# Optimization experiments

Measured on AMD Instinct MI355X. Metric: run time of the kernel, lower is better.

## Reference

```python
import math
import jax, jax.numpy as jnp
import numpy as np

B, CK, H, W = 4, 64, 48, 84


def setup_inputs() -> dict:
    key = jax.random.key(0)
    k1, k2 = jax.random.split(key)
    mk = jax.random.normal(k1, (B, CK, 1, H, W), dtype=jnp.float32)
    qk = jax.random.normal(k2, (B, CK, H, W), dtype=jnp.float32)
    return {"mk": mk, "qk": qk}


def reference(mk, qk):
    b_, ck = mk.shape[0], mk.shape[1]
    mkf = mk.reshape(b_, ck, -1)            # [B, CK, N]  (N = T*H*W, T=1)
    qkf = qk.reshape(b_, ck, -1)            # [B, CK, M]  (M = H*W)
    a = jnp.sum(mkf * mkf, axis=1)[:, :, None]              # [B, N, 1]
    b = 2.0 * jnp.einsum('bcn,bcm->bnm', mkf, qkf)          # [B, N, M]
    c = jnp.sum(qkf * qkf, axis=1)[:, None, :]              # [B, 1, M]
    affinity = (-a + b - c) / math.sqrt(ck)                 # -||mk - qk||^2 / sqrt(CK)
    return jax.nn.softmax(affinity, axis=1)                 # softmax over memory axis
```

## Files before the change

kernel.cpp:

```cpp
#include <hip/hip_runtime.h>
#include <math.h>

#define B_  4
#define CK_ 64
#define N_  4032
#define M_  4032
#define NP_ 4096
#define MP_ 4096

#define P1C 8
#define P1T 8
#define P2G 8
#define P2T 8

typedef __attribute__((ext_vector_type(8))) short short8;
typedef __attribute__((ext_vector_type(4))) float float4v;

__device__ inline unsigned short f2bf(float x) {
    unsigned u = __float_as_uint(x);
    u += 0x7FFF + ((u >> 16) & 1);
    return (unsigned short)(u >> 16);
}
__device__ inline float bf2f(unsigned short h) {
    return __uint_as_float(((unsigned)h) << 16);
}

__global__ __launch_bounds__(256) void prep_kernel(
    const float* __restrict__ mk, const float* __restrict__ qk,
    unsigned short* __restrict__ mk_hi, unsigned short* __restrict__ mk_lo,
    unsigned short* __restrict__ qk_hi, unsigned short* __restrict__ qk_lo,
    float* __restrict__ u)
{
    __shared__ float tile[64][65];
    __shared__ float sred[4][64];
    const int t  = threadIdx.x;
    const int n0 = blockIdx.x * 64;
    const int b  = blockIdx.y;
    const int which = blockIdx.z;
    const bool pad = (n0 >= N_);

    const float* src = (which == 0 ? mk : qk) + (size_t)b * CK_ * N_;
    unsigned short* dhi = (which == 0 ? mk_hi : qk_hi) + (size_t)b * NP_ * CK_;
    unsigned short* dlo = (which == 0 ? mk_lo : qk_lo) + (size_t)b * NP_ * CK_;

    if (!pad) {
        #pragma unroll
        for (int i = 0; i < 16; ++i) {
            const int idx = t + 256 * i;
            const int c = idx >> 6, n = idx & 63;
            tile[c][n] = src[(size_t)c * N_ + n0 + n];
        }
    } else {
        #pragma unroll
        for (int i = 0; i < 16; ++i) {
            const int idx = t + 256 * i;
            tile[idx >> 6][idx & 63] = 0.f;
        }
    }
    __syncthreads();

    const int n = t & 63;
    const int g = t >> 6;
    unsigned short hbits[16], lbits[16];
    float ssq = 0.f;
    #pragma unroll
    for (int i = 0; i < 16; ++i) {
        const float x = tile[g * 16 + i][n];
        const unsigned short h = f2bf(x);
        hbits[i] = h;
        lbits[i] = f2bf(x - bf2f(h));
        ssq = fmaf(x, x, ssq);
    }
    {
        union { short8 v; unsigned short s[8]; } p0, p1, q0, q1;
        #pragma unroll
        for (int i = 0; i < 8; ++i) {
            p0.s[i] = hbits[i]; p1.s[i] = hbits[8 + i];
            q0.s[i] = lbits[i]; q1.s[i] = lbits[8 + i];
        }
        const size_t base = (size_t)(n0 + n) * CK_ + g * 16;
        *(short8*)(dhi + base)     = p0.v;
        *(short8*)(dhi + base + 8) = p1.v;
        *(short8*)(dlo + base)     = q0.v;
        *(short8*)(dlo + base + 8) = q1.v;
    }
    sred[g][n] = ssq;
    __syncthreads();
    if (which == 0 && t < 64) {
        const float tot = sred[0][t] + sred[1][t] + sred[2][t] + sred[3][t];
        u[(size_t)b * NP_ + n0 + t] = pad ? 0.f : __expf(-0.125f * tot);
    }
}


__global__ __launch_bounds__(512) void pass1_kernel(
    const unsigned short* __restrict__ mk_hi, const unsigned short* __restrict__ mk_lo,
    const unsigned short* __restrict__ qk_hi, const unsigned short* __restrict__ qk_lo,
    const float* __restrict__ u, float* __restrict__ psum)
{
    __shared__ float cs[2][128];
    const int t = threadIdx.x;
    const int wave = t >> 6, lane = t & 63;
    const int wn = wave & 1, wm = wave >> 1;
    const int lcol = lane & 15;
    const int quad = lane >> 4;
    const int chunk = blockIdx.y;
    const int b = blockIdx.z;
    const int m_base = blockIdx.x * 128 + wm * 32;

    const unsigned short* mh = mk_hi + (size_t)b * NP_ * CK_;
    const unsigned short* ml = mk_lo + (size_t)b * NP_ * CK_;
    const unsigned short* qh = qk_hi + (size_t)b * NP_ * CK_;
    const unsigned short* ql = qk_lo + (size_t)b * NP_ * CK_;
    const float* ub = u + (size_t)b * NP_;

    short8 bh[2][2], bl[2][2];
    #pragma unroll
    for (int cg = 0; cg < 2; ++cg) {
        const size_t mrow = (size_t)(m_base + cg * 16 + lcol) * CK_;
        #pragma unroll
        for (int kc = 0; kc < 2; ++kc) {
            const size_t off = mrow + kc * 32 + quad * 8;
            bh[cg][kc] = *(const short8*)(qh + off);
            bl[cg][kc] = *(const short8*)(ql + off);
        }
    }

    float p0 = 0.f, p1 = 0.f;

    #pragma unroll 2
    for (int it = chunk * P1T; it < chunk * P1T + P1T; ++it) {
        const int n_base = it * 64 + wn * 32;
        short8 ah[2][2], al[2][2];
        #pragma unroll
        for (int rg = 0; rg < 2; ++rg) {
            const size_t nrow = (size_t)(n_base + rg * 16 + lcol) * CK_;
            #pragma unroll
            for (int kc = 0; kc < 2; ++kc) {
                const size_t off = nrow + kc * 32 + quad * 8;
                ah[rg][kc] = *(const short8*)(mh + off);
                al[rg][kc] = *(const short8*)(ml + off);
            }
        }
        float4v uv0 = *(const float4v*)(ub + n_base + quad * 4);
        float4v uv1 = *(const float4v*)(ub + n_base + 16 + quad * 4);

        #pragma unroll
        for (int rg = 0; rg < 2; ++rg) {
            #pragma unroll
            for (int cg = 0; cg < 2; ++cg) {
                float4v a1 = {0.f, 0.f, 0.f, 0.f};
                float4v a2 = {0.f, 0.f, 0.f, 0.f};
                __builtin_amdgcn_s_setprio(1);
                #pragma unroll
                for (int kc = 0; kc < 2; ++kc) {
                    a1 = __builtin_amdgcn_mfma_f32_16x16x32_bf16(ah[rg][kc], bh[cg][kc], a1, 0, 0, 0);
                    a2 = __builtin_amdgcn_mfma_f32_16x16x32_bf16(ah[rg][kc], bl[cg][kc], a2, 0, 0, 0);
                    a2 = __builtin_amdgcn_mfma_f32_16x16x32_bf16(al[rg][kc], bh[cg][kc], a2, 0, 0, 0);
                }
                __builtin_amdgcn_s_setprio(0);
                float ps = 0.f;
                #pragma unroll
                for (int r = 0; r < 4; ++r) {
                    const float dot = a1[r] + a2[r];
                    const float uvr = (rg == 0) ? uv0[r] : uv1[r];
                    ps += uvr * __expf(0.25f * dot);
                }
                if (cg == 0) p0 += ps; else p1 += ps;
            }
        }
    }

    p0 += __shfl_xor(p0, 16); p0 += __shfl_xor(p0, 32);
    p1 += __shfl_xor(p1, 16); p1 += __shfl_xor(p1, 32);
    if (lane < 16) {
        cs[wn][wm * 32 + lcol]      = p0;
        cs[wn][wm * 32 + 16 + lcol] = p1;
    }
    __syncthreads();
    if (t < 128) {
        psum[((size_t)b * P1C + chunk) * MP_ + blockIdx.x * 128 + t] =
            cs[0][t] + cs[1][t];
    }
}

__global__ __launch_bounds__(512) void pass2_kernel(
    const unsigned short* __restrict__ mk_hi, const unsigned short* __restrict__ mk_lo,
    const unsigned short* __restrict__ qk_hi, const unsigned short* __restrict__ qk_lo,
    const float* __restrict__ u, const float* __restrict__ psum,
    float* __restrict__ out)
{
    const int t = threadIdx.x;
    const int wave = t >> 6, lane = t & 63;
    const int wn = wave & 1, wm = wave >> 1;
    const int lcol = lane & 15;
    const int quad = lane >> 4;
    const int b = blockIdx.z;
    const int m_base = blockIdx.x * 128 + wm * 32;

    const unsigned short* mh = mk_hi + (size_t)b * NP_ * CK_;
    const unsigned short* ml = mk_lo + (size_t)b * NP_ * CK_;
    const unsigned short* qh = qk_hi + (size_t)b * NP_ * CK_;
    const unsigned short* ql = qk_lo + (size_t)b * NP_ * CK_;
    const float* ub = u + (size_t)b * NP_;

    short8 qah[2][2], qal[2][2];
    #pragma unroll
    for (int mg = 0; mg < 2; ++mg) {
        const size_t mrow = (size_t)(m_base + mg * 16 + lcol) * CK_;
        #pragma unroll
        for (int kc = 0; kc < 2; ++kc) {
            const size_t off = mrow + kc * 32 + quad * 8;
            qah[mg][kc] = *(const short8*)(qh + off);
            qal[mg][kc] = *(const short8*)(ql + off);
        }
    }

    float4v rinv4[2];
    #pragma unroll
    for (int mg = 0; mg < 2; ++mg) {
        float4v tot = {0.f, 0.f, 0.f, 0.f};
        #pragma unroll
        for (int c = 0; c < P1C; ++c) {
            const float4v p = *(const float4v*)(
                psum + ((size_t)b * P1C + c) * MP_ + m_base + mg * 16 + quad * 4);
            tot += p;
        }
        rinv4[mg][0] = 1.f / tot[0];
        rinv4[mg][1] = 1.f / tot[1];
        rinv4[mg][2] = 1.f / tot[2];
        rinv4[mg][3] = 1.f / tot[3];
    }

    const bool mval0 = (m_base < N_);
    const bool mval1 = (m_base + 16 < N_);

    float* obase = out + (size_t)b * N_ * M_ + m_base + quad * 4;

    #pragma unroll 2
    for (int j = 0; j < P2T; ++j) {
        const int n_base = (blockIdx.y * P2T + j) * 64 + wn * 32;

        short8 bh[2][2], bl[2][2];
        #pragma unroll
        for (int ng = 0; ng < 2; ++ng) {
            const size_t nrow = (size_t)(n_base + ng * 16 + lcol) * CK_;
            #pragma unroll
            for (int kc = 0; kc < 2; ++kc) {
                const size_t off = nrow + kc * 32 + quad * 8;
                bh[ng][kc] = *(const short8*)(mh + off);
                bl[ng][kc] = *(const short8*)(ml + off);
            }
        }
        float un[2];
        #pragma unroll
        for (int ng = 0; ng < 2; ++ng)
            un[ng] = ub[n_base + ng * 16 + lcol];

        const bool nval = (n_base < N_);

        #pragma unroll
        for (int mg = 0; mg < 2; ++mg) {
            #pragma unroll
            for (int ng = 0; ng < 2; ++ng) {
                float4v a1 = {0.f, 0.f, 0.f, 0.f};
                float4v a2 = {0.f, 0.f, 0.f, 0.f};
                __builtin_amdgcn_s_setprio(1);
                #pragma unroll
                for (int kc = 0; kc < 2; ++kc) {
                    a1 = __builtin_amdgcn_mfma_f32_16x16x32_bf16(qah[mg][kc], bh[ng][kc], a1, 0, 0, 0);
                    a2 = __builtin_amdgcn_mfma_f32_16x16x32_bf16(qah[mg][kc], bl[ng][kc], a2, 0, 0, 0);
                    a2 = __builtin_amdgcn_mfma_f32_16x16x32_bf16(qal[mg][kc], bh[ng][kc], a2, 0, 0, 0);
                }
                __builtin_amdgcn_s_setprio(0);
                float4v v;
                #pragma unroll
                for (int r = 0; r < 4; ++r) {
                    const float dot = a1[r] + a2[r];
                    v[r] = un[ng] * __expf(0.25f * dot) * rinv4[mg][r];
                }
                if (nval && (mg == 0 ? mval0 : mval1)) {
                    float4v* dst = (float4v*)(
                        obase + (size_t)(n_base + ng * 16 + lcol) * M_ + mg * 16);
                    __builtin_nontemporal_store(v, dst);
                }
            }
        }
    }
}

extern "C" void kernel_launch(void* const* d_in, const int* in_sizes, int n_in,
                              void* d_out, int out_size, void* d_ws, size_t ws_size,
                              hipStream_t stream) {
    const float* mk = (const float*)d_in[0];
    const float* qk = (const float*)d_in[1];
    float* out = (float*)d_out;

    unsigned short* mk_hi = (unsigned short*)d_ws;
    unsigned short* mk_lo = mk_hi + (size_t)B_ * NP_ * CK_;
    unsigned short* qk_hi = mk_lo + (size_t)B_ * NP_ * CK_;
    unsigned short* qk_lo = qk_hi + (size_t)B_ * NP_ * CK_;
    float* u    = (float*)(qk_lo + (size_t)B_ * NP_ * CK_);
    float* psum = u + (size_t)B_ * NP_;

    prep_kernel<<<dim3(NP_ / 64, B_, 2), 256, 0, stream>>>(mk, qk, mk_hi, mk_lo, qk_hi, qk_lo, u);
    pass1_kernel<<<dim3(MP_ / 128, P1C, B_), 512, 0, stream>>>(mk_hi, mk_lo, qk_hi, qk_lo, u, psum);
    pass2_kernel<<<dim3(MP_ / 128, P2G, B_), 512, 0, stream>>>(mk_hi, mk_lo, qk_hi, qk_lo, u, psum, out);
}
```

Measured before the change: 377.2 us.

## Fuse softmax passes: one GEMM pass writing fp16 weights, then in-place normalise

The second GEMM-plus-exp pass is gone. Pass1 now computes the unnormalised weights u·exp(dot/4)·v once, stores them as fp16 in the first half of each output row, and accumulates the per-column partial sums. A small reduce kernel turns the partials into reciprocals, and a streaming pass2 reads the fp16 row and writes the scaled fp32 result back in place. This halves the MFMA and exp work, at the cost of an extra fp16 write and read of the whole matrix. It also risks precision loss, because the tiny unnormalised weights fall into the fp16 subnormal range.

```diff
diff --git a/kernel.cpp b/kernel.cpp
--- a/kernel.cpp
+++ b/kernel.cpp
@@ -1,4 +1,5 @@
 #include <hip/hip_runtime.h>
+#include <hip/hip_fp16.h>
 #include <math.h>
 
 #define B_  4
@@ -10,8 +11,6 @@
 
 #define P1C 8
 #define P1T 8
-#define P2G 8
-#define P2T 8
 
 typedef __attribute__((ext_vector_type(8))) short short8;
 typedef __attribute__((ext_vector_type(4))) float float4v;
@@ -29,7 +28,7 @@
     const float* __restrict__ mk, const float* __restrict__ qk,
     unsigned short* __restrict__ mk_hi, unsigned short* __restrict__ mk_lo,
     unsigned short* __restrict__ qk_hi, unsigned short* __restrict__ qk_lo,
-    float* __restrict__ u)
+    float* __restrict__ u, float* __restrict__ v)
 {
     __shared__ float tile[64][65];
     __shared__ float sred[4][64];
@@ -72,23 +71,24 @@
         ssq = fmaf(x, x, ssq);
     }
     {
-        union { short8 v; unsigned short s[8]; } p0, p1, q0, q1;
+        union { short8 vv; unsigned short s[8]; } p0, p1, q0, q1;
         #pragma unroll
         for (int i = 0; i < 8; ++i) {
             p0.s[i] = hbits[i]; p1.s[i] = hbits[8 + i];
             q0.s[i] = lbits[i]; q1.s[i] = lbits[8 + i];
         }
         const size_t base = (size_t)(n0 + n) * CK_ + g * 16;
-        *(short8*)(dhi + base)     = p0.v;
-        *(short8*)(dhi + base + 8) = p1.v;
-        *(short8*)(dlo + base)     = q0.v;
-        *(short8*)(dlo + base + 8) = q1.v;
+        *(short8*)(dhi + base)     = p0.vv;
+        *(short8*)(dhi + base + 8) = p1.vv;
+        *(short8*)(dlo + base)     = q0.vv;
+        *(short8*)(dlo + base + 8) = q1.vv;
     }
     sred[g][n] = ssq;
     __syncthreads();
-    if (which == 0 && t < 64) {
+    if (t < 64) {
         const float tot = sred[0][t] + sred[1][t] + sred[2][t] + sred[3][t];
-        u[(size_t)b * NP_ + n0 + t] = pad ? 0.f : __expf(-0.125f * tot);
+        float* dst = (which == 0 ? u : v);
+        dst[(size_t)b * NP_ + n0 + t] = pad ? 0.f : __expf(-0.125f * tot);
     }
 }
 
@@ -96,7 +96,8 @@
 __global__ __launch_bounds__(512) void pass1_kernel(
     const unsigned short* __restrict__ mk_hi, const unsigned short* __restrict__ mk_lo,
     const unsigned short* __restrict__ qk_hi, const unsigned short* __restrict__ qk_lo,
-    const float* __restrict__ u, float* __restrict__ psum)
+    const float* __restrict__ u, const float* __restrict__ v,
+    float* __restrict__ psum, float* __restrict__ out)
 {
     __shared__ float cs[2][128];
     const int t = threadIdx.x;
@@ -114,96 +115,6 @@
     const unsigned short* ql = qk_lo + (size_t)b * NP_ * CK_;
     const float* ub = u + (size_t)b * NP_;
 
-    short8 bh[2][2], bl[2][2];
-    #pragma unroll
-    for (int cg = 0; cg < 2; ++cg) {
-        const size_t mrow = (size_t)(m_base + cg * 16 + lcol) * CK_;
-        #pragma unroll
-        for (int kc = 0; kc < 2; ++kc) {
-            const size_t off = mrow + kc * 32 + quad * 8;
-            bh[cg][kc] = *(const short8*)(qh + off);
-            bl[cg][kc] = *(const short8*)(ql + off);
-        }
-    }
-
-    float p0 = 0.f, p1 = 0.f;
-
-    #pragma unroll 2
-    for (int it = chunk * P1T; it < chunk * P1T + P1T; ++it) {
-        const int n_base = it * 64 + wn * 32;
-        short8 ah[2][2], al[2][2];
-        #pragma unroll
-        for (int rg = 0; rg < 2; ++rg) {
-            const size_t nrow = (size_t)(n_base + rg * 16 + lcol) * CK_;
-            #pragma unroll
-            for (int kc = 0; kc < 2; ++kc) {
-                const size_t off = nrow + kc * 32 + quad * 8;
-                ah[rg][kc] = *(const short8*)(mh + off);
-                al[rg][kc] = *(const short8*)(ml + off);
-            }
-        }
-        float4v uv0 = *(const float4v*)(ub + n_base + quad * 4);
-        float4v uv1 = *(const float4v*)(ub + n_base + 16 + quad * 4);
-
-        #pragma unroll
-        for (int rg = 0; rg < 2; ++rg) {
-            #pragma unroll
-            for (int cg = 0; cg < 2; ++cg) {
-                float4v a1 = {0.f, 0.f, 0.f, 0.f};
-                float4v a2 = {0.f, 0.f, 0.f, 0.f};
-                __builtin_amdgcn_s_setprio(1);
-                #pragma unroll
-                for (int kc = 0; kc < 2; ++kc) {
-                    a1 = __builtin_amdgcn_mfma_f32_16x16x32_bf16(ah[rg][kc], bh[cg][kc], a1, 0, 0, 0);
-                    a2 = __builtin_amdgcn_mfma_f32_16x16x32_bf16(ah[rg][kc], bl[cg][kc], a2, 0, 0, 0);
-                    a2 = __builtin_amdgcn_mfma_f32_16x16x32_bf16(al[rg][kc], bh[cg][kc], a2, 0, 0, 0);
-                }
-                __builtin_amdgcn_s_setprio(0);
-                float ps = 0.f;
-                #pragma unroll
-                for (int r = 0; r < 4; ++r) {
-                    const float dot = a1[r] + a2[r];
-                    const float uvr = (rg == 0) ? uv0[r] : uv1[r];
-                    ps += uvr * __expf(0.25f * dot);
-                }
-                if (cg == 0) p0 += ps; else p1 += ps;
-            }
-        }
-    }
-
-    p0 += __shfl_xor(p0, 16); p0 += __shfl_xor(p0, 32);
-    p1 += __shfl_xor(p1, 16); p1 += __shfl_xor(p1, 32);
-    if (lane < 16) {
-        cs[wn][wm * 32 + lcol]      = p0;
-        cs[wn][wm * 32 + 16 + lcol] = p1;
-    }
-    __syncthreads();
-    if (t < 128) {
-        psum[((size_t)b * P1C + chunk) * MP_ + blockIdx.x * 128 + t] =
-            cs[0][t] + cs[1][t];
-    }
-}
-
-__global__ __launch_bounds__(512) void pass2_kernel(
-    const unsigned short* __restrict__ mk_hi, const unsigned short* __restrict__ mk_lo,
-    const unsigned short* __restrict__ qk_hi, const unsigned short* __restrict__ qk_lo,
-    const float* __restrict__ u, const float* __restrict__ psum,
-    float* __restrict__ out)
-{
-    const int t = threadIdx.x;
-    const int wave = t >> 6, lane = t & 63;
-    const int wn = wave & 1, wm = wave >> 1;
-    const int lcol = lane & 15;
-    const int quad = lane >> 4;
-    const int b = blockIdx.z;
-    const int m_base = blockIdx.x * 128 + wm * 32;
-
-    const unsigned short* mh = mk_hi + (size_t)b * NP_ * CK_;
-    const unsigned short* ml = mk_lo + (size_t)b * NP_ * CK_;
-    const unsigned short* qh = qk_hi + (size_t)b * NP_ * CK_;
-    const unsigned short* ql = qk_lo + (size_t)b * NP_ * CK_;
-    const float* ub = u + (size_t)b * NP_;
-
     short8 qah[2][2], qal[2][2];
     #pragma unroll
     for (int mg = 0; mg < 2; ++mg) {
@@ -216,30 +127,25 @@
         }
     }
 
-    float4v rinv4[2];
-    #pragma unroll
-    for (int mg = 0; mg < 2; ++mg) {
-        float4v tot = {0.f, 0.f, 0.f, 0.f};
-        #pragma unroll
-        for (int c = 0; c < P1C; ++c) {
-            const float4v p = *(const float4v*)(
-                psum + ((size_t)b * P1C + c) * MP_ + m_base + mg * 16 + quad * 4);
-            tot += p;
-        }
-        rinv4[mg][0] = 1.f / tot[0];
-        rinv4[mg][1] = 1.f / tot[1];
-        rinv4[mg][2] = 1.f / tot[2];
-        rinv4[mg][3] = 1.f / tot[3];
-    }
-
-    const bool mval0 = (m_base < N_);
-    const bool mval1 = (m_base + 16 < N_);
-
-    float* obase = out + (size_t)b * N_ * M_ + m_base + quad * 4;
+    float4v vv[2];
+    #pragma unroll
+    for (int mg = 0; mg < 2; ++mg)
+        vv[mg] = *(const float4v*)(v + (size_t)b * NP_ + m_base + mg * 16 + quad * 4);
+
+    const bool mv0 = (m_base < N_);
+    const bool mv1 = (m_base + 16 < N_);
+
+    unsigned short* wb = (unsigned short*)(out + (size_t)b * N_ * M_);
+
+    float ps[2][4];
+    #pragma unroll
+    for (int mg = 0; mg < 2; ++mg)
+        #pragma unroll
+        for (int r = 0; r < 4; ++r) ps[mg][r] = 0.f;
 
     #pragma unroll 2
-    for (int j = 0; j < P2T; ++j) {
-        const int n_base = (blockIdx.y * P2T + j) * 64 + wn * 32;
+    for (int it = chunk * P1T; it < chunk * P1T + P1T; ++it) {
+        const int n_base = it * 64 + wn * 32;
 
         short8 bh[2][2], bl[2][2];
         #pragma unroll
@@ -252,12 +158,13 @@
                 bl[ng][kc] = *(const short8*)(ml + off);
             }
         }
-        float un[2];
+        float un_[2];
         #pragma unroll
         for (int ng = 0; ng < 2; ++ng)
-            un[ng] = ub[n_base + ng * 16 + lcol];
-
-        const bool nval = (n_base < N_);
+            un_[ng] = ub[n_base + ng * 16 + lcol];
+
+        const bool nv0 = (n_base < N_);
+        const bool nv1 = (n_base + 16 < N_);
 
         #pragma unroll
         for (int mg = 0; mg < 2; ++mg) {
@@ -273,19 +180,114 @@
                     a2 = __builtin_amdgcn_mfma_f32_16x16x32_bf16(qal[mg][kc], bh[ng][kc], a2, 0, 0, 0);
                 }
                 __builtin_amdgcn_s_setprio(0);
-                float4v v;
+                float4v wv;
                 #pragma unroll
                 for (int r = 0; r < 4; ++r) {
                     const float dot = a1[r] + a2[r];
-                    v[r] = un[ng] * __expf(0.25f * dot) * rinv4[mg][r];
+                    wv[r] = un_[ng] * __expf(0.25f * dot) * vv[mg][r];
+                    ps[mg][r] += wv[r];
                 }
-                if (nval && (mg == 0 ? mval0 : mval1)) {
-                    float4v* dst = (float4v*)(
-                        obase + (size_t)(n_base + ng * 16 + lcol) * M_ + mg * 16);
-                    __builtin_nontemporal_store(v, dst);
+                if ((ng == 0 ? nv0 : nv1) && (mg == 0 ? mv0 : mv1)) {
+                    __half2 hA = __floats2half2_rn(wv[0], wv[1]);
+                    __half2 hB = __floats2half2_rn(wv[2], wv[3]);
+                    uint2 pk;
+                    pk.x = *(unsigned*)&hA;
+                    pk.y = *(unsigned*)&hB;
+                    *(uint2*)(wb + (size_t)(n_base + ng * 16 + lcol) * (2 * M_)
+                                  + m_base + mg * 16 + quad * 4) = pk;
                 }
             }
         }
+    }
+
+    #pragma unroll
+    for (int mg = 0; mg < 2; ++mg)
+        #pragma unroll
+        for (int r = 0; r < 4; ++r) {
+            float s = ps[mg][r];
+            s += __shfl_xor(s, 1);
+            s += __shfl_xor(s, 2);
+            s += __shfl_xor(s, 4);
+            s += __shfl_xor(s, 8);
+            ps[mg][r] = s;
+        }
+    if (lcol == 0) {
+        #pragma unroll
+        for (int mg = 0; mg < 2; ++mg)
+            #pragma unroll
+            for (int r = 0; r < 4; ++r)
+                cs[wn][wm * 32 + mg * 16 + quad * 4 + r] = ps[mg][r];
+    }
+    __syncthreads();
+    if (t < 128) {
+        psum[((size_t)b * P1C + chunk) * MP_ + blockIdx.x * 128 + t] =
+            cs[0][t] + cs[1][t];
+    }
+}
+
+__global__ __launch_bounds__(256) void reduce_kernel(
+    const float* __restrict__ psum, float* __restrict__ rinv)
+{
+    const int m = blockIdx.x * 256 + threadIdx.x;
+    const int b = blockIdx.y;
+    float s = 0.f;
+    #pragma unroll
+    for (int c = 0; c < P1C; ++c)
+        s += psum[((size_t)b * P1C + c) * MP_ + m];
+    rinv[(size_t)b * MP_ + m] = 1.f / s;
+}
+
+__global__ __launch_bounds__(256) void pass2_kernel(
+    const float* __restrict__ rinv, float* __restrict__ out)
+{
+    const int t = threadIdx.x;
+    const int n = blockIdx.x;
+    const int b = blockIdx.y;
+    float* row = out + ((size_t)b * N_ + n) * M_;
+    const unsigned short* wr = (const unsigned short*)row;
+    const float* rv = rinv + (size_t)b * MP_;
+
+    const int c0 = t;
+    const int c1 = t + 256;
+    const bool has1 = (c1 < (M_ / 8));
+
+    uint4 q0 = *(const uint4*)(wr + c0 * 8);
+    float4v ra0 = *(const float4v*)(rv + c0 * 8);
+    float4v rb0 = *(const float4v*)(rv + c0 * 8 + 4);
+    uint4 q1;
+    float4v ra1, rb1;
+    if (has1) {
+        q1  = *(const uint4*)(wr + c1 * 8);
+        ra1 = *(const float4v*)(rv + c1 * 8);
+        rb1 = *(const float4v*)(rv + c1 * 8 + 4);
+    }
+
+    float4v xa0, xb0, xa1, xb1;
+    {
+        float2 f0 = __half22float2(*(const __half2*)&q0.x);
+        float2 f1 = __half22float2(*(const __half2*)&q0.y);
+        float2 f2 = __half22float2(*(const __half2*)&q0.z);
+        float2 f3 = __half22float2(*(const __half2*)&q0.w);
+        xa0 = (float4v){f0.x * ra0[0], f0.y * ra0[1], f1.x * ra0[2], f1.y * ra0[3]};
+        xb0 = (float4v){f2.x * rb0[0], f2.y * rb0[1], f3.x * rb0[2], f3.y * rb0[3]};
+    }
+    if (has1) {
+        float2 f0 = __half22float2(*(const __half2*)&q1.x);
+        float2 f1 = __half22float2(*(const __half2*)&q1.y);
+        float2 f2 = __half22float2(*(const __half2*)&q1.z);
+        float2 f3 = __half22float2(*(const __half2*)&q1.w);
+        xa1 = (float4v){f0.x * ra1[0], f0.y * ra1[1], f1.x * ra1[2], f1.y * ra1[3]};
+        xb1 = (float4v){f2.x * rb1[0], f2.y * rb1[1], f3.x * rb1[2], f3.y * rb1[3]};
+    }
+
+    asm volatile("s_waitcnt vmcnt(0)" ::: "memory");
+    __syncthreads();
+
+    __builtin_nontemporal_store(xa0, (float4v*)(row + c0 * 8));
+    __builtin_nontemporal_store(xb0, (float4v*)(row + c0 * 8 + 4));
+    if (has1) {
+        __builtin_nontemporal_store(xa1, (float4v*)(row + c1 * 8));
+        __builtin_nontemporal_store(xb1, (float4v*)(row + c1 * 8 + 4));
     }
 }
 
@@ -301,9 +303,12 @@
     unsigned short* qk_hi = mk_lo + (size_t)B_ * NP_ * CK_;
     unsigned short* qk_lo = qk_hi + (size_t)B_ * NP_ * CK_;
     float* u    = (float*)(qk_lo + (size_t)B_ * NP_ * CK_);
-    float* psum = u + (size_t)B_ * NP_;
-
-    prep_kernel<<<dim3(NP_ / 64, B_, 2), 256, 0, stream>>>(mk, qk, mk_hi, mk_lo, qk_hi, qk_lo, u);
-    pass1_kernel<<<dim3(MP_ / 128, P1C, B_), 512, 0, stream>>>(mk_hi, mk_lo, qk_hi, qk_lo, u, psum);
-    pass2_kernel<<<dim3(MP_ / 128, P2G, B_), 512, 0, stream>>>(mk_hi, mk_lo, qk_hi, qk_lo, u, psum, out);
-}
+    float* v    = u + (size_t)B_ * NP_;
+    float* psum = v + (size_t)B_ * NP_;
+    float* rinv = psum + (size_t)B_ * P1C * MP_;
+
+    prep_kernel<<<dim3(NP_ / 64, B_, 2), 256, 0, stream>>>(mk, qk, mk_hi, mk_lo, qk_hi, qk_lo, u, v);
+    pass1_kernel<<<dim3(MP_ / 128, P1C, B_), 512, 0, stream>>>(mk_hi, mk_lo, qk_hi, qk_lo, u, v, psum, out);
+    reduce_kernel<<<dim3(MP_ / 256, B_), 256, 0, stream>>>(psum, rinv);
+    pass2_kernel<<<dim3(N_, B_), 256, 0, stream>>>(rinv, out);
+}
```

After: 382.1 us. Within noise of the previous version (+1.3%).
